# Kernel optimization log

Hardware: AMD Instinct MI355X
Metric: run time of the kernel (lower is better)

The kernel has to match this reference:

```python
import jax, jax.numpy as jnp
import numpy as np

D_MODEL = 2048
NUM_HEADS = 16
NUM_KV_HEADS = 4
HEAD_DIM = D_MODEL // NUM_HEADS
ROPE_THETA = 10000.0


def setup_inputs() -> dict:
    key = jax.random.key(0)
    ks = jax.random.split(key, 5)
    B, S = 2, 2048
    scale = 0.02
    return {
        "x": jax.random.normal(ks[0], (B, S, D_MODEL), dtype=jnp.float32),
        "wq": jax.random.normal(ks[1], (D_MODEL, NUM_HEADS * HEAD_DIM), dtype=jnp.float32) * scale,
        "wk": jax.random.normal(ks[2], (D_MODEL, NUM_KV_HEADS * HEAD_DIM), dtype=jnp.float32) * scale,
        "wv": jax.random.normal(ks[3], (D_MODEL, NUM_KV_HEADS * HEAD_DIM), dtype=jnp.float32) * scale,
        "wo": jax.random.normal(ks[4], (NUM_HEADS * HEAD_DIM, D_MODEL), dtype=jnp.float32) * scale,
    }


def _rope_cos_sin(seq_len, head_dim, dtype):
    # Llama-style: freqs over even indices, angles = pos * inv_freq
    inv_freq = 1.0 / (ROPE_THETA ** (jnp.arange(0, head_dim, 2, dtype=jnp.float32) / head_dim))
    ang = jnp.arange(seq_len, dtype=jnp.float32)[:, None] * inv_freq[None, :]  # [S, hd/2]
    cos = jnp.cos(ang).astype(dtype)[None, :, None, :]  # [1,S,1,hd/2]
    sin = jnp.sin(ang).astype(dtype)[None, :, None, :]
    return cos, sin


def _apply_rope(x, cos, sin):
    # x: [B,S,H,hd]; interleaved complex rotation on pairs (x[2i], x[2i+1])
    x1 = x[..., 0::2]
    x2 = x[..., 1::2]
    y1 = x1 * cos - x2 * sin
    y2 = x1 * sin + x2 * cos
    return jnp.stack([y1, y2], axis=-1).reshape(x.shape)


def reference(x, wq, wk, wv, wo):
    B, S, D = x.shape
    H, KV, hd = NUM_HEADS, NUM_KV_HEADS, HEAD_DIM
    g = H // KV
    q = (x @ wq).reshape(B, S, H, hd)
    k = (x @ wk).reshape(B, S, KV, hd)
    v = (x @ wv).reshape(B, S, KV, hd)
    cos, sin = _rope_cos_sin(S, hd, x.dtype)
    q = _apply_rope(q, cos, sin)
    k = _apply_rope(k, cos, sin)
    q = q.transpose(0, 2, 1, 3)  # [B,H,S,hd]
    k = k.transpose(0, 2, 1, 3)  # [B,KV,S,hd]
    v = v.transpose(0, 2, 1, 3)
    k = jnp.repeat(k, g, axis=1)  # GQA: [B,H,S,hd]
    v = jnp.repeat(v, g, axis=1)
    attn = jnp.einsum('bqsh,bqlh->bqsl', q, k) * (1.0 / np.sqrt(hd)).astype(np.float32)
    attn = jax.nn.softmax(attn, axis=-1)  # non-causal, as in source
    out = jnp.einsum('bqsl,bqlh->bqsh', attn, v)
    out = out.transpose(0, 2, 1, 3).reshape(B, S, D)
    return out @ wo
```

## Files before the change

### kernel.cpp

```cpp
#include <hip/hip_runtime.h>


typedef __attribute__((ext_vector_type(8))) short short8;
typedef __attribute__((ext_vector_type(4))) float f32x4;

#define DEV static __device__ __forceinline__

#define NB 2
#define NS 2048
#define ND 2048
#define NH 16
#define NKV 4
#define HD 128
#define NQKV 3072

DEV unsigned short f2bf(float f) {
  union { float f; unsigned u; } v; v.f = f;
  unsigned r = v.u + 0x7fffu + ((v.u >> 16) & 1u);
  return (unsigned short)(r >> 16);
}
DEV unsigned short f2bf_fast(float f) {
  union { float f; unsigned u; } v; v.f = f;
  return (unsigned short)((v.u + 0x8000u) >> 16);
}
DEV float bf2f(unsigned short u) {
  union { unsigned u; float f; } v; v.u = ((unsigned)u) << 16; return v.f;
}
DEV unsigned pack2bf(float a, float b) {
  return (unsigned)f2bf_fast(a) | ((unsigned)f2bf_fast(b) << 16);
}
DEV unsigned pack2bf_rne(float a, float b) {
  return (unsigned)f2bf(a) | ((unsigned)f2bf(b) << 16);
}

DEV void swap32(unsigned &x, unsigned &y) {
  asm volatile("v_permlane32_swap_b32 %0, %1" : "+v"(x), "+v"(y));
}
DEV void swap16(unsigned &x, unsigned &y) {
  asm volatile("v_permlane16_swap_b32 %0, %1" : "+v"(x), "+v"(y));
}

typedef const __attribute__((address_space(1))) void* gas1_t;
typedef __attribute__((address_space(3))) void* las3_t;
DEV void gload16(const void* g, void* l) {
  __builtin_amdgcn_global_load_lds((gas1_t)g, (las3_t)l, 16, 0, 0);
}

DEV f32x4 mfma16(short8 a, short8 b, f32x4 c) {
  return __builtin_amdgcn_mfma_f32_16x16x32_bf16(a, b, c, 0, 0, 0);
}


__global__ __launch_bounds__(256) void convert_x_kernel(const float* __restrict__ x,
                                                        unsigned short* __restrict__ xb) {
  size_t i = ((size_t)blockIdx.x * 256 + threadIdx.x) * 4;
  float4 v = *(const float4*)(x + i);
  unsigned long long pack = (unsigned long long)f2bf(v.x)
                          | ((unsigned long long)f2bf(v.y) << 16)
                          | ((unsigned long long)f2bf(v.z) << 32)
                          | ((unsigned long long)f2bf(v.w) << 48);
  *(unsigned long long*)(xb + i) = pack;
}

__global__ __launch_bounds__(256) void transpose_w_kernel(const float* __restrict__ src,
                                                          unsigned short* __restrict__ dst,
                                                          int K, int N) {
  __shared__ float tile[64][65];
  const int k0 = blockIdx.x * 64, n0 = blockIdx.y * 64;
  for (int i = threadIdx.x; i < 4096; i += 256) {
    int r = i >> 6, c = i & 63;
    tile[r][c] = src[(size_t)(k0 + r) * N + n0 + c];
  }
  __syncthreads();
  for (int i = threadIdx.x; i < 4096; i += 256) {
    int r = i >> 6, c = i & 63;
    dst[(size_t)(n0 + r) * K + k0 + c] = f2bf(tile[c][r]);
  }
}

__global__ __launch_bounds__(256) void rope_table_kernel(float2* __restrict__ tab) {
  int t = blockIdx.x * 256 + threadIdx.x;
  int s = t >> 6, i = t & 63;
  float freq = powf(10000.0f, -(float)i * (1.0f / 64.0f));
  float ang = (float)s * freq;
  tab[t] = make_float2(cosf(ang), sinf(ang));
}

__global__ __launch_bounds__(256) void rope_scatter_kernel(const unsigned short* __restrict__ QKV,
                                                           const float2* __restrict__ tab,
                                                           unsigned short* __restrict__ Qb,
                                                           unsigned short* __restrict__ Kb) {
  int t = blockIdx.x * 256 + threadIdx.x;
  const float qscale = 0.12751741161895452f;
  if (t < (1 << 22)) {
    int i = t & 63, h = (t >> 6) & 15, s = (t >> 10) & 2047, b = t >> 21;
    const unsigned short* p = QKV + (size_t)(b * NS + s) * NQKV + h * HD + 2 * i;
    float2 cs = tab[s * 64 + i];
    float x1 = bf2f(p[0]), x2 = bf2f(p[1]);
    unsigned short* q = Qb + (size_t)((b * NH + h) * NS + s) * HD + 2 * i;
    q[0] = f2bf((x1 * cs.x - x2 * cs.y) * qscale);
    q[1] = f2bf((x1 * cs.y + x2 * cs.x) * qscale);
  } else {
    int u = t - (1 << 22);
    int i = u & 63, kv = (u >> 6) & 3, s = (u >> 8) & 2047, b = u >> 19;
    const unsigned short* p = QKV + (size_t)(b * NS + s) * NQKV + 2048 + kv * HD + 2 * i;
    float2 cs = tab[s * 64 + i];
    float x1 = bf2f(p[0]), x2 = bf2f(p[1]);
    unsigned short* k = Kb + (size_t)((b * NKV + kv) * NS + s) * HD + 2 * i;
    k[0] = f2bf(x1 * cs.x - x2 * cs.y);
    k[1] = f2bf(x1 * cs.y + x2 * cs.x);
  }
}

__global__ __launch_bounds__(256) void transpose_v_kernel(const unsigned short* __restrict__ QKV,
                                                          unsigned short* __restrict__ Vt) {
  __shared__ unsigned short tile[64][65];
  const int bk = blockIdx.x, b = bk >> 2, kv = bk & 3;
  const int s0 = blockIdx.y * 64, d0 = blockIdx.z * 64;
  for (int i = threadIdx.x; i < 4096; i += 256) {
    int r = i >> 6, c = i & 63;
    tile[r][c] = QKV[(size_t)(b * NS + s0 + r) * NQKV + 2560 + kv * HD + d0 + c];
  }
  __syncthreads();
  for (int i = threadIdx.x; i < 4096; i += 256) {
    int r = i >> 6, c = i & 63;
    Vt[(size_t)((b * NKV + kv) * HD + d0 + r) * NS + s0 + c] = tile[c][r];
  }
}


template <int N, bool OUTBF16>
__global__ __launch_bounds__(256) void gemm_kernel(const unsigned short* __restrict__ A,
                                                   const unsigned short* __restrict__ Bt,
                                                   void* __restrict__ Cout) {
  __shared__ unsigned short As[128 * 32];
  __shared__ unsigned short Bs[128 * 32];
  const int K = 2048;
  const int tid = threadIdx.x, wid = tid >> 6, lane = tid & 63;
  const int wm = wid >> 1, wn = wid & 1;
  const int m0 = blockIdx.x * 128, n0 = blockIdx.y * 128;
  f32x4 acc[4][4] = {};
  const int srow = tid >> 2;
  const int scol = (tid & 3) * 8;
  const unsigned short* Ab = A + (size_t)(m0 + srow) * K + scol;
  const unsigned short* Ab2 = Ab + (size_t)64 * K;
  const unsigned short* Bb = Bt + (size_t)(n0 + srow) * K + scol;
  const unsigned short* Bb2 = Bb + (size_t)64 * K;

  for (int kt = 0; kt < K; kt += 32) {
    gload16(Ab + kt, &As[wid * 512]);
    gload16(Ab2 + kt, &As[2048 + wid * 512]);
    gload16(Bb + kt, &Bs[wid * 512]);
    gload16(Bb2 + kt, &Bs[2048 + wid * 512]);
    __syncthreads();
    short8 af[4], bfr[4];
#pragma unroll
    for (int r = 0; r < 4; ++r)
      af[r] = *(const short8*)&As[(wm * 64 + r * 16 + (lane & 15)) * 32 + (lane >> 4) * 8];
#pragma unroll
    for (int c = 0; c < 4; ++c)
      bfr[c] = *(const short8*)&Bs[(wn * 64 + c * 16 + (lane & 15)) * 32 + (lane >> 4) * 8];
    __builtin_amdgcn_s_setprio(1);
#pragma unroll
    for (int r = 0; r < 4; ++r)
#pragma unroll
      for (int c = 0; c < 4; ++c)
        acc[r][c] = mfma16(af[r], bfr[c], acc[r][c]);
    __builtin_amdgcn_s_setprio(0);
    __syncthreads();
  }

  if (OUTBF16) {
    unsigned short* C = (unsigned short*)Cout;
#pragma unroll
    for (int r = 0; r < 4; ++r) {
      const int row = m0 + wm * 64 + r * 16 + (lane >> 4) * 4;
#pragma unroll
      for (int c = 0; c < 4; ++c) {
        const int col = n0 + wn * 64 + c * 16 + (lane & 15);
#pragma unroll
        for (int j = 0; j < 4; ++j)
          C[(size_t)(row + j) * N + col] = f2bf(acc[r][c][j]);
      }
    }
  } else {
    float* C = (float*)Cout;
#pragma unroll
    for (int r = 0; r < 4; ++r) {
      const int row = m0 + wm * 64 + r * 16 + (lane >> 4) * 4;
#pragma unroll
      for (int c = 0; c < 4; ++c) {
        const int col = n0 + wn * 64 + c * 16 + (lane & 15);
#pragma unroll
        for (int j = 0; j < 4; ++j)
          C[(size_t)(row + j) * N + col] = acc[r][c][j];
      }
    }
  }
}


__global__ __launch_bounds__(256, 2) void attn_kernel(const unsigned short* __restrict__ Qb,
                                                      const unsigned short* __restrict__ Kb,
                                                      const unsigned short* __restrict__ Vt,
                                                      unsigned short* __restrict__ O) {
  __shared__ unsigned short Ks[2][64 * 128];
  __shared__ unsigned short Vs[2][128 * 64];
  const int tid = threadIdx.x, wid = tid >> 6, lane = tid & 63;
  const int blk = blockIdx.x;
  const int qt = blk & 15, h = (blk >> 4) & 15, b = blk >> 8;
  const int kvh = h >> 2;
  const int q0 = qt * 128 + wid * 32;

  const unsigned short* qhead = Qb + (size_t)((b * NH + h) * NS) * HD;
  const unsigned short* khead = Kb + (size_t)((b * NKV + kvh) * NS) * HD;
  const unsigned short* vhead = Vt + (size_t)((b * NKV + kvh) * HD) * NS;

  const int cl = lane & 15, g4 = (lane >> 4) * 4, hi8 = (lane >> 4) * 8;
  const int swk = (lane & 7) << 3;

  auto stageKV = [&](int buf, int kt) {
#pragma unroll
    for (int i = 0; i < 4; ++i) {
      int row = i * 16 + (tid >> 4);
      int col = ((tid & 15) * 8) ^ ((row & 7) << 3);
      gload16(khead + (size_t)(kt + row) * HD + col, &Ks[buf][i * 2048 + wid * 512]);
    }
#pragma unroll
    for (int i = 0; i < 4; ++i) {
      int row = i * 32 + (tid >> 3);
      int col = ((tid & 7) * 8) ^ ((row & 7) << 3);
      gload16(vhead + (size_t)row * NS + kt + col, &Vs[buf][i * 2048 + wid * 512]);
    }
  };

  stageKV(0, 0);

  short8 qf[2][4];
#pragma unroll
  for (int r = 0; r < 2; ++r)
#pragma unroll
    for (int kk = 0; kk < 4; ++kk)
      qf[r][kk] = *(const short8*)(qhead + (size_t)(q0 + r * 16 + cl) * HD + kk * 32 + hi8);

  f32x4 od[2][8] = {};
  float mrun[2] = {-1e30f, -1e30f}, lpart[2] = {0.f, 0.f};

  int cur = 0;
  for (int it = 0; it < NS / 64; ++it) {
    if (it + 1 < NS / 64) {
      stageKV(cur ^ 1, (it + 1) * 64);
      asm volatile("s_waitcnt vmcnt(8)" ::: "memory");
    } else {
      asm volatile("s_waitcnt vmcnt(0)" ::: "memory");
    }
    __builtin_amdgcn_s_barrier();

    const unsigned short* ks = Ks[cur];
    const unsigned short* vs = Vs[cur];

    f32x4 s[2][4];
#pragma unroll
    for (int r = 0; r < 2; ++r)
#pragma unroll
      for (int c4 = 0; c4 < 4; ++c4) s[r][c4] = f32x4{0.f, 0.f, 0.f, 0.f};
    __builtin_amdgcn_s_setprio(1);
#pragma unroll
    for (int c4 = 0; c4 < 4; ++c4)
#pragma unroll
      for (int kk = 0; kk < 4; ++kk) {
        short8 kf = *(const short8*)&ks[((c4 * 16 + cl) * 128 + kk * 32 + hi8) ^ swk];
        s[0][c4] = mfma16(kf, qf[0][kk], s[0][c4]);
        s[1][c4] = mfma16(kf, qf[1][kk], s[1][c4]);
      }
    __builtin_amdgcn_s_setprio(0);

    float mt[2];
#pragma unroll
    for (int r = 0; r < 2; ++r) {
      float m = fmaxf(fmaxf(fmaxf(s[r][0][0], s[r][0][1]), fmaxf(s[r][0][2], s[r][0][3])),
                      fmaxf(fmaxf(s[r][1][0], s[r][1][1]), fmaxf(s[r][1][2], s[r][1][3])));
      float m2 = fmaxf(fmaxf(fmaxf(s[r][2][0], s[r][2][1]), fmaxf(s[r][2][2], s[r][2][3])),
                       fmaxf(fmaxf(s[r][3][0], s[r][3][1]), fmaxf(s[r][3][2], s[r][3][3])));
      m = fmaxf(m, m2);
      m = fmaxf(m, __shfl_xor(m, 16, 64));
      m = fmaxf(m, __shfl_xor(m, 32, 64));
      mt[r] = m;
    }
    bool need = (mt[0] > mrun[0] + 8.0f) || (mt[1] > mrun[1] + 8.0f);
    if (__any(need)) {
#pragma unroll
      for (int r = 0; r < 2; ++r) {
        float mn = fmaxf(mrun[r], mt[r]);
        float corr = __builtin_amdgcn_exp2f(mrun[r] - mn);
        mrun[r] = mn;
        lpart[r] *= corr;
#pragma unroll
        for (int c = 0; c < 8; ++c)
          od[r][c] *= corr;
      }
    }
#pragma unroll
    for (int r = 0; r < 2; ++r) {
      float acc = 0.f;
#pragma unroll
      for (int c4 = 0; c4 < 4; ++c4)
#pragma unroll
        for (int j = 0; j < 4; ++j) {
          float p = __builtin_amdgcn_exp2f(s[r][c4][j] - mrun[r]);
          s[r][c4][j] = p;
          acc += p;
        }
      lpart[r] += acc;
    }

    short8 pb[2][2];
#pragma unroll
    for (int r = 0; r < 2; ++r) {
      unsigned w00 = pack2bf(s[r][0][0], s[r][0][1]), w01 = pack2bf(s[r][0][2], s[r][0][3]);
      unsigned w10 = pack2bf(s[r][1][0], s[r][1][1]), w11 = pack2bf(s[r][1][2], s[r][1][3]);
      unsigned w20 = pack2bf(s[r][2][0], s[r][2][1]), w21 = pack2bf(s[r][2][2], s[r][2][3]);
      unsigned w30 = pack2bf(s[r][3][0], s[r][3][1]), w31 = pack2bf(s[r][3][2], s[r][3][3]);
      union { unsigned u[4]; short8 v; } t0, t1;
      swap32(w00, w10); swap16(w00, w10); t0.u[0] = w00; t0.u[2] = w10;
      swap32(w01, w11); swap16(w01, w11); t0.u[1] = w01; t0.u[3] = w11;
      swap32(w20, w30); swap16(w20, w30); t1.u[0] = w20; t1.u[2] = w30;
      swap32(w21, w31); swap16(w21, w31); t1.u[1] = w21; t1.u[3] = w31;
      pb[r][0] = t0.v;
      pb[r][1] = t1.v;
    }

    __builtin_amdgcn_s_setprio(1);
#pragma unroll
    for (int c = 0; c < 8; ++c) {
      const int rr = c * 16 + cl;
      short8 vf0 = *(const short8*)&vs[(rr * 64 + hi8) ^ swk];
      short8 vf1 = *(const short8*)&vs[(rr * 64 + 32 + hi8) ^ swk];
      od[0][c] = mfma16(vf0, pb[0][0], od[0][c]);
      od[0][c] = mfma16(vf1, pb[0][1], od[0][c]);
      od[1][c] = mfma16(vf0, pb[1][0], od[1][c]);
      od[1][c] = mfma16(vf1, pb[1][1], od[1][c]);
    }
    __builtin_amdgcn_s_setprio(0);
    __builtin_amdgcn_s_barrier();
    cur ^= 1;
  }

  float linv[2];
#pragma unroll
  for (int r = 0; r < 2; ++r) {
    float l = lpart[r];
    l += __shfl_xor(l, 16, 64);
    l += __shfl_xor(l, 32, 64);
    linv[r] = 1.0f / l;
  }
#pragma unroll
  for (int r = 0; r < 2; ++r) {
    const size_t row = (size_t)(b * NS + q0 + 16 * r + cl);
#pragma unroll
    for (int c = 0; c < 8; ++c) {
      uint2 pk;
      pk.x = pack2bf_rne(od[r][c][0] * linv[r], od[r][c][1] * linv[r]);
      pk.y = pack2bf_rne(od[r][c][2] * linv[r], od[r][c][3] * linv[r]);
      *(uint2*)(O + row * ND + h * HD + c * 16 + g4) = pk;
    }
  }
}


extern "C" void kernel_launch(void* const* d_in, const int* in_sizes, int n_in,
                              void* d_out, int out_size, void* d_ws, size_t ws_size,
                              hipStream_t stream) {
  const float* x  = (const float*)d_in[0];
  const float* wq = (const float*)d_in[1];
  const float* wk = (const float*)d_in[2];
  const float* wv = (const float*)d_in[3];
  const float* wo = (const float*)d_in[4];
  float* out = (float*)d_out;
  char* ws = (char*)d_ws;

  unsigned short* xb   = (unsigned short*)(ws + 0);
  unsigned short* wT   = (unsigned short*)(ws + 16777216);
  unsigned short* woT  = (unsigned short*)(ws + 29360128);
  float2*         tab  = (float2*)(ws + 37748736);
  unsigned short* QKV  = (unsigned short*)(ws + 38797312);
  unsigned short* Qb   = xb;
  unsigned short* Kb   = wT;
  unsigned short* Vt   = (unsigned short*)(ws + 16777216 + 4194304);
  unsigned short* Obuf = QKV;

  convert_x_kernel<<<8192, 256, 0, stream>>>(x, xb);
  transpose_w_kernel<<<dim3(32, 32), 256, 0, stream>>>(wq, wT, 2048, 2048);
  transpose_w_kernel<<<dim3(32, 8),  256, 0, stream>>>(wk, wT + (size_t)2048 * 2048, 2048, 512);
  transpose_w_kernel<<<dim3(32, 8),  256, 0, stream>>>(wv, wT + (size_t)2560 * 2048, 2048, 512);
  transpose_w_kernel<<<dim3(32, 32), 256, 0, stream>>>(wo, woT, 2048, 2048);
  rope_table_kernel<<<512, 256, 0, stream>>>(tab);

  gemm_kernel<NQKV, true><<<dim3(32, 24), 256, 0, stream>>>(xb, wT, QKV);

  rope_scatter_kernel<<<20480, 256, 0, stream>>>(QKV, tab, Qb, Kb);
  transpose_v_kernel<<<dim3(8, 32, 2), 256, 0, stream>>>(QKV, Vt);

  attn_kernel<<<512, 256, 0, stream>>>(Qb, Kb, Vt, Obuf);

  gemm_kernel<ND, false><<<dim3(32, 16), 256, 0, stream>>>(Obuf, woT, out);
}
```

Before: 248.4 us.

## Load V fragments directly from global memory and use hardware bf16 pack

Drops LDS staging of the transposed V tile. Each wave now loads its V fragments straight from global memory (via L2/L1) into registers after the QK matmul, and only K is double-buffered in LDS. This cuts LDS footprint and global-to-LDS traffic, and the explicit vmcnt waits are replaced by __syncthreads. The manual float-to-bf16 packing is replaced with the v_cvt_pk_bf16_f32 instruction. The risks are exposed global-load latency on V, since the loads are issued only shortly before the PV MFMAs, redundant V reads across the four waves, and more VGPRs to hold 16 V fragments.

After: 291.7 us. 17.4% more time.

```diff
diff --git a/kernel.cpp b/kernel.cpp
--- a/kernel.cpp
+++ b/kernel.cpp
@@ -19,18 +19,16 @@
   unsigned r = v.u + 0x7fffu + ((v.u >> 16) & 1u);
   return (unsigned short)(r >> 16);
 }
-DEV unsigned short f2bf_fast(float f) {
-  union { float f; unsigned u; } v; v.f = f;
-  return (unsigned short)((v.u + 0x8000u) >> 16);
-}
 DEV float bf2f(unsigned short u) {
   union { unsigned u; float f; } v; v.u = ((unsigned)u) << 16; return v.f;
 }
-DEV unsigned pack2bf(float a, float b) {
-  return (unsigned)f2bf_fast(a) | ((unsigned)f2bf_fast(b) << 16);
-}
 DEV unsigned pack2bf_rne(float a, float b) {
   return (unsigned)f2bf(a) | ((unsigned)f2bf(b) << 16);
+}
+DEV unsigned cvtpk(float a, float b) {
+  unsigned r;
+  asm("v_cvt_pk_bf16_f32 %0, %1, %2" : "=v"(r) : "v"(a), "v"(b));
+  return r;
 }
 
 DEV void swap32(unsigned &x, unsigned &y) {
@@ -205,7 +203,6 @@
                                                       const unsigned short* __restrict__ Vt,
                                                       unsigned short* __restrict__ O) {
   __shared__ unsigned short Ks[2][64 * 128];
-  __shared__ unsigned short Vs[2][128 * 64];
   const int tid = threadIdx.x, wid = tid >> 6, lane = tid & 63;
   const int blk = blockIdx.x;
   const int qt = blk & 15, h = (blk >> 4) & 15, b = blk >> 8;
@@ -219,22 +216,16 @@
   const int cl = lane & 15, g4 = (lane >> 4) * 4, hi8 = (lane >> 4) * 8;
   const int swk = (lane & 7) << 3;
 
-  auto stageKV = [&](int buf, int kt) {
+  auto stageK = [&](int buf, int kt) {
 #pragma unroll
     for (int i = 0; i < 4; ++i) {
       int row = i * 16 + (tid >> 4);
       int col = ((tid & 15) * 8) ^ ((row & 7) << 3);
       gload16(khead + (size_t)(kt + row) * HD + col, &Ks[buf][i * 2048 + wid * 512]);
     }
-#pragma unroll
-    for (int i = 0; i < 4; ++i) {
-      int row = i * 32 + (tid >> 3);
-      int col = ((tid & 7) * 8) ^ ((row & 7) << 3);
-      gload16(vhead + (size_t)row * NS + kt + col, &Vs[buf][i * 2048 + wid * 512]);
-    }
   };
 
-  stageKV(0, 0);
+  stageK(0, 0);
 
   short8 qf[2][4];
 #pragma unroll
@@ -246,18 +237,14 @@
   f32x4 od[2][8] = {};
   float mrun[2] = {-1e30f, -1e30f}, lpart[2] = {0.f, 0.f};
 
+  __syncthreads();
+
   int cur = 0;
   for (int it = 0; it < NS / 64; ++it) {
-    if (it + 1 < NS / 64) {
-      stageKV(cur ^ 1, (it + 1) * 64);
-      asm volatile("s_waitcnt vmcnt(8)" ::: "memory");
-    } else {
-      asm volatile("s_waitcnt vmcnt(0)" ::: "memory");
-    }
-    __builtin_amdgcn_s_barrier();
+    const int kt = it * 64;
+    if (it + 1 < NS / 64) stageK(cur ^ 1, kt + 64);
 
     const unsigned short* ks = Ks[cur];
-    const unsigned short* vs = Vs[cur];
 
     f32x4 s[2][4];
 #pragma unroll
@@ -274,6 +261,14 @@
         s[1][c4] = mfma16(kf, qf[1][kk], s[1][c4]);
       }
     __builtin_amdgcn_s_setprio(0);
+
+    short8 vfa[8], vfb[8];
+#pragma unroll
+    for (int c = 0; c < 8; ++c) {
+      const unsigned short* vrow = vhead + (size_t)(c * 16 + cl) * NS + kt + hi8;
+      vfa[c] = *(const short8*)(vrow);
+      vfb[c] = *(const short8*)(vrow + 32);
+    }
 
     float mt[2];
 #pragma unroll
@@ -317,10 +312,10 @@
     short8 pb[2][2];
 #pragma unroll
     for (int r = 0; r < 2; ++r) {
-      unsigned w00 = pack2bf(s[r][0][0], s[r][0][1]), w01 = pack2bf(s[r][0][2], s[r][0][3]);
-      unsigned w10 = pack2bf(s[r][1][0], s[r][1][1]), w11 = pack2bf(s[r][1][2], s[r][1][3]);
-      unsigned w20 = pack2bf(s[r][2][0], s[r][2][1]), w21 = pack2bf(s[r][2][2], s[r][2][3]);
-      unsigned w30 = pack2bf(s[r][3][0], s[r][3][1]), w31 = pack2bf(s[r][3][2], s[r][3][3]);
+      unsigned w00 = cvtpk(s[r][0][0], s[r][0][1]), w01 = cvtpk(s[r][0][2], s[r][0][3]);
+      unsigned w10 = cvtpk(s[r][1][0], s[r][1][1]), w11 = cvtpk(s[r][1][2], s[r][1][3]);
+      unsigned w20 = cvtpk(s[r][2][0], s[r][2][1]), w21 = cvtpk(s[r][2][2], s[r][2][3]);
+      unsigned w30 = cvtpk(s[r][3][0], s[r][3][1]), w31 = cvtpk(s[r][3][2], s[r][3][3]);
       union { unsigned u[4]; short8 v; } t0, t1;
       swap32(w00, w10); swap16(w00, w10); t0.u[0] = w00; t0.u[2] = w10;
       swap32(w01, w11); swap16(w01, w11); t0.u[1] = w01; t0.u[3] = w11;
@@ -333,16 +328,14 @@
     __builtin_amdgcn_s_setprio(1);
 #pragma unroll
     for (int c = 0; c < 8; ++c) {
-      const int rr = c * 16 + cl;
-      short8 vf0 = *(const short8*)&vs[(rr * 64 + hi8) ^ swk];
-      short8 vf1 = *(const short8*)&vs[(rr * 64 + 32 + hi8) ^ swk];
-      od[0][c] = mfma16(vf0, pb[0][0], od[0][c]);
-      od[0][c] = mfma16(vf1, pb[0][1], od[0][c]);
-      od[1][c] = mfma16(vf0, pb[1][0], od[1][c]);
-      od[1][c] = mfma16(vf1, pb[1][1], od[1][c]);
+      od[0][c] = mfma16(vfa[c], pb[0][0], od[0][c]);
+      od[0][c] = mfma16(vfb[c], pb[0][1], od[0][c]);
+      od[1][c] = mfma16(vfa[c], pb[1][0], od[1][c]);
+      od[1][c] = mfma16(vfb[c], pb[1][1], od[1][c]);
     }
     __builtin_amdgcn_s_setprio(0);
-    __builtin_amdgcn_s_barrier();
+
+    __syncthreads();
     cur ^= 1;
   }
 
```
